# Performance work log

Hardware: AMD Instinct MI355X
Metric: run time of the kernel (lower is better)

Reference implementation:

```python
import jax, jax.numpy as jnp
import numpy as np

B, N, D = 32, 2048, 1024


def setup_inputs() -> dict:
    key = jax.random.key(0)
    k1, k2, k3, k4, k5, k6 = jax.random.split(key, 6)
    encoded = jax.random.normal(k1, (B, N, D), dtype=jnp.float32)
    decoder_state = jax.random.normal(k2, (B, D), dtype=jnp.float32)
    mask = jax.random.randint(k3, (B, N), 0, 2, dtype=jnp.int32)
    scale = 1.0 / np.sqrt(D)
    W1 = jax.random.normal(k4, (D, D), dtype=jnp.float32) * scale  # applied as x @ W1
    W2 = jax.random.normal(k5, (D, D), dtype=jnp.float32) * scale
    vt = jax.random.normal(k6, (D,), dtype=jnp.float32) * scale
    return {"encoded": encoded, "decoder_state": decoder_state, "mask": mask,
            "W1": W1, "W2": W2, "vt": vt}


def reference(encoded, decoder_state, mask, W1, W2, vt):
    temperature = 1.0
    # process_encoded: W1(encoded)  [B, N, D]
    enc = jnp.einsum('bnd,de->bne', encoded, W1)
    # W2(decoder_state)  [B, D] -> broadcast-add over N
    dec = decoder_state @ W2
    # vt(tanh(.)).squeeze(2)  -> logits [B, N]
    u = jnp.einsum('bnd,d->bn', jnp.tanh(enc + dec[:, None, :]), vt)
    # masked log-softmax with temperature over dim=1
    logits = u / temperature + jnp.log(mask.astype(u.dtype) + 1e-45)
    return jax.nn.log_softmax(logits, axis=1)
```

## Files before the change

### kernel.cpp

```cpp
#include <hip/hip_runtime.h>

typedef _Float16 half8 __attribute__((ext_vector_type(8)));
typedef _Float16 half4 __attribute__((ext_vector_type(4)));
typedef __fp16   pk2   __attribute__((ext_vector_type(2)));
typedef float    f32x4 __attribute__((ext_vector_type(4)));

#define GLOBAL_AS __attribute__((address_space(1)))
#define LDS_AS    __attribute__((address_space(3)))

static constexpr int Bb = 32;
static constexpr int Nn = 2048;
static constexpr int Dd = 1024;
static constexpr int M  = Bb * Nn;


__global__ void prep_w1(const float* __restrict__ W1, _Float16* __restrict__ W1TT) {
    int g = blockIdx.x * 256 + threadIdx.x;
    int chunk = g >> 10;
    int u = g & 1023;
    int q = u >> 7, sc = u & 127;
    int cl = sc ^ (2 * (q & 3));
    int et = chunk >> 5, t = (chunk >> 1) & 15, h = chunk & 1;
    int e  = et * 256 + h * 128 + cl;
    int k0 = t * 64 + q * 8;
    half8 hh;
#pragma unroll
    for (int j = 0; j < 8; ++j)
        hh[j] = (_Float16)W1[(size_t)(k0 + j) * Dd + e];
    *(half8*)(W1TT + (size_t)g * 8) = hh;
}

__global__ void dec_kernel(const float* __restrict__ ds, const float* __restrict__ W2,
                           float* __restrict__ dec) {
    __shared__ float part[4][64];
    int b = blockIdx.x, ech = blockIdx.y;
    int tid = threadIdx.x;
    int e = ech * 64 + (tid & 63);
    int dc = tid >> 6;
    float acc = 0.f;
#pragma unroll 4
    for (int d = dc * 256; d < dc * 256 + 256; ++d)
        acc += ds[b * Dd + d] * W2[(size_t)d * Dd + e];
    part[dc][tid & 63] = acc;
    __syncthreads();
    if (tid < 64)
        dec[b * Dd + e] = part[0][tid] + part[1][tid] + part[2][tid] + part[3][tid];
}

#define BAR     asm volatile("s_barrier" ::: "memory")
#define LGKM(n) asm volatile("s_waitcnt lgkmcnt(" #n ")" ::: "memory")
#define VM(n)   asm volatile("s_waitcnt vmcnt(" #n ")" ::: "memory")
#define PRIO1   __builtin_amdgcn_s_setprio(1)
#define PRIO0   __builtin_amdgcn_s_setprio(0)

#define RD_A(dst, base) do { _Pragma("unroll") \
  for (int ks = 0; ks < 2; ++ks) { \
    _Pragma("unroll") for (int m2 = 0; m2 < 4; ++m2) { \
      const int row_ = m2 * 32 + rA; \
      const int kc0_ = (ks * 4 + qq) * 2; \
      dst[m2][ks] = *(const half8*)&lds[(base) + (row_ * 16 + (kc0_ ^ rxa)) * 4]; \
    } } } while (0)

#define RD_B(dst, base) do { _Pragma("unroll") \
  for (int ks = 0; ks < 2; ++ks) { const int qb = ((ks * 4 + qq) * 128) * 8; \
    _Pragma("unroll") for (int j2 = 0; j2 < 2; ++j2) \
      dst[j2][ks] = *(const half8*)&lds[(base) + qb + (j2 * 64 + rB) * 8]; } } while (0)

#define MFMAQ(A_, B_, ro, co) do { \
  _Pragma("unroll") for (int m2 = 0; m2 < 4; ++m2) \
  _Pragma("unroll") for (int j2 = 0; j2 < 2; ++j2) { \
    acc[(ro) + m2][(co) + j2] = __builtin_amdgcn_mfma_f32_16x16x32_f16( \
        A_[m2][0], B_[j2][0], acc[(ro) + m2][(co) + j2], 0, 0, 0); \
    acc[(ro) + m2][(co) + j2] = __builtin_amdgcn_mfma_f32_16x16x32_f16( \
        A_[m2][1], B_[j2][1], acc[(ro) + m2][(co) + j2], 0, 0, 0); } } while (0)

__global__ __launch_bounds__(512, 2) void gemm8(
    const float* __restrict__ encA, const _Float16* __restrict__ W1TT,
    const float* __restrict__ dec, const float* __restrict__ vt,
    float* __restrict__ u_part)
{
    extern __shared__ _Float16 lds[];

    const int g  = blockIdx.x;
    const int wg = (g & 7) * 128 + (g >> 3);
    const int et    = wg & 3;
    const int mtile = wg >> 2;

    const int tid  = threadIdx.x;
    const int lane = tid & 63, wid = tid >> 6;
    const int wr = wid >> 2, wc = wid & 3;
    const int qq = lane >> 4, l15 = lane & 15;
    const int l15s = l15 ^ (2 * qq);
    const int rA = wr * 16 + l15;
    const int rxa = (l15 & 7) * 2;
    const int rB = wc * 16 + l15s;

    f32x4 acc[8][4] = {};
    half8 a[4][2], b0[2][2], b1[2][2];
    f32x4 aSt[8];

    const int arow0 = tid >> 4;
    const int l16   = tid & 15;
    const float* agp = encA + (((size_t)(mtile * 256 + arow0)) << 10) + l16 * 4;

    const size_t bbase = (size_t)et * 32 * 8192;
    const int uoff = tid * 8;

    auto issueA = [&](int T) {
        const float* gp = agp + T * 64;
#pragma unroll
        for (int p = 0; p < 8; ++p)
            aSt[p] = *(const f32x4*)(gp + ((size_t)p << 15));
    };
    auto writeA = [&](int Tn) {
        const int base = (Tn & 1) << 14;
#pragma unroll
        for (int p = 0; p < 8; ++p) {
            const int rf = p * 32 + arow0;
            const int h  = rf >> 7, row = rf & 127;
            pk2 c0 = __builtin_amdgcn_cvt_pkrtz(aSt[p][0], aSt[p][1]);
            pk2 c1 = __builtin_amdgcn_cvt_pkrtz(aSt[p][2], aSt[p][3]);
            half4 hh; hh[0] = c0[0]; hh[1] = c0[1]; hh[2] = c1[0]; hh[3] = c1[1];
            *(half4*)&lds[base + h * 8192
                          + (row * 16 + (l16 ^ ((row & 7) * 2))) * 4] = hh;
        }
    };
    auto stB = [&](int T, int h) {
        const _Float16* gp = W1TT + bbase + ((size_t)(T * 2 + h) << 13) + uoff;
        _Float16* lp = lds + (32768 + (((T & 1) * 2 + h) << 13) + (wid << 9));
        __builtin_amdgcn_global_load_lds((const GLOBAL_AS void*)gp,
                                         (LDS_AS void*)lp, 16, 0, 0);
        __builtin_amdgcn_global_load_lds((const GLOBAL_AS void*)(gp + 4096),
                                         (LDS_AS void*)(lp + 4096), 16, 0, 0);
    };


    issueA(0); stB(0, 0); stB(0, 1);
    VM(4);
    writeA(0);
    VM(0); LGKM(0);
    BAR;

#pragma unroll 2
    for (int T = 0; T < 16; ++T) {
        const int As  = (T & 1) << 14;
        const int Bs2 = 32768 + ((T & 1) << 14);
        const bool s = (T < 15);

        if (s) { issueA(T + 1); stB(T + 1, 0); stB(T + 1, 1); }

        RD_A(a, As);
        RD_B(b0, Bs2);
        RD_B(b1, Bs2 + 8192);
        LGKM(4);
        PRIO1; MFMAQ(a, b0, 0, 0); PRIO0;
        LGKM(0);
        PRIO1; MFMAQ(a, b1, 0, 2); PRIO0;
        RD_A(a, As + 8192);
        LGKM(0);
        PRIO1; MFMAQ(a, b0, 4, 0); MFMAQ(a, b1, 4, 2); PRIO0;

        if (s) { VM(4); writeA(T + 1); }
        VM(0); LGKM(0);
        BAR;
    }

    const int b = mtile >> 3;
    float vtv[4], dcv[4];
#pragma unroll
    for (int nf = 0; nf < 4; ++nf) {
        int e = et * 256 + (nf >> 1) * 128 + (nf & 1) * 64 + wc * 16 + l15;
        vtv[nf] = vt[e];
        dcv[nf] = dec[b * Dd + e];
    }
    float* usum = (float*)lds;
#pragma unroll
    for (int hm = 0; hm < 8; ++hm) {
        const int h = hm >> 2, mq = hm & 3;
#pragma unroll
        for (int r = 0; r < 4; ++r) {
            float sv = 0.f;
#pragma unroll
            for (int nf = 0; nf < 4; ++nf) {
                float x  = acc[hm][nf][r] + dcv[nf];
                float ex = __expf(2.f * x);
                sv += (1.f - 2.f * __builtin_amdgcn_rcpf(ex + 1.f)) * vtv[nf];
            }
#pragma unroll
            for (int off = 1; off < 16; off <<= 1) sv += __shfl_xor(sv, off, 16);
            if (l15 == 0)
                usum[wc * 256 + h * 128 + mq * 32 + wr * 16 + qq * 4 + r] = sv;
        }
    }
    __syncthreads();
    if (tid < 256) {
        float v = usum[tid] + usum[256 + tid] + usum[512 + tid] + usum[768 + tid];
        u_part[(size_t)et * M + (size_t)mtile * 256 + tid] = v;
    }
}

__global__ void softmax_k(const float* __restrict__ up, const int* __restrict__ mask,
                          float* __restrict__ out) {
    __shared__ float red[8];
    int b = blockIdx.x, tid = threadIdx.x;
    float l[8];
#pragma unroll
    for (int i = 0; i < 8; ++i) {
        int n = i * 256 + tid;
        float s = up[(size_t)b * Nn + n];
#pragma unroll
        for (int et = 1; et < 4; ++et) s += up[(size_t)et * M + (size_t)b * Nn + n];
        l[i] = s + (mask[b * Nn + n] ? 0.f : -103.278931f);
    }
    float m = l[0];
#pragma unroll
    for (int i = 1; i < 8; ++i) m = fmaxf(m, l[i]);
#pragma unroll
    for (int o = 32; o >= 1; o >>= 1) m = fmaxf(m, __shfl_xor(m, o, 64));
    if ((tid & 63) == 0) red[tid >> 6] = m;
    __syncthreads();
    m = fmaxf(fmaxf(red[0], red[1]), fmaxf(red[2], red[3]));
    float s = 0.f;
#pragma unroll
    for (int i = 0; i < 8; ++i) s += expf(l[i] - m);
#pragma unroll
    for (int o = 32; o >= 1; o >>= 1) s += __shfl_xor(s, o, 64);
    if ((tid & 63) == 0) red[4 + (tid >> 6)] = s;
    __syncthreads();
    float lse = m + logf(red[4] + red[5] + red[6] + red[7]);
#pragma unroll
    for (int i = 0; i < 8; ++i)
        out[(size_t)b * Nn + i * 256 + tid] = l[i] - lse;
}

extern "C" void kernel_launch(void* const* d_in, const int* in_sizes, int n_in,
                              void* d_out, int out_size, void* d_ws, size_t ws_size,
                              hipStream_t stream) {
    const float* encoded = (const float*)d_in[0];
    const float* dstate  = (const float*)d_in[1];
    const int*   mask    = (const int*)d_in[2];
    const float* W1      = (const float*)d_in[3];
    const float* W2      = (const float*)d_in[4];
    const float* vt      = (const float*)d_in[5];
    float* out = (float*)d_out;

    char* ws = (char*)d_ws;
    float*    u_part = (float*)ws;
    float*    dec    = (float*)(ws + (size_t)4 * M * 4);
    _Float16* W1TT   = (_Float16*)(ws + (size_t)4 * M * 4 + (size_t)Bb * Dd * 4);

    static bool attr_done = false;
    if (!attr_done) {
        hipFuncSetAttribute(reinterpret_cast<const void*>(gemm8),
                            hipFuncAttributeMaxDynamicSharedMemorySize, 131072);
        attr_done = true;
    }

    prep_w1<<<512, 256, 0, stream>>>(W1, W1TT);
    dec_kernel<<<dim3(32, 16), 256, 0, stream>>>(dstate, W2, dec);
    gemm8<<<1024, 512, 131072, stream>>>(encoded, W1TT, dec, vt, u_part);
    softmax_k<<<32, 256, 0, stream>>>(u_part, mask, out);
}
```

Baseline: 523.7 us.

## Split A-tile staging into two halves to cut registers and overlap with MFMA

The fp32 A-tile prefetch is split into two halves of four vectors each. The first half is written to LDS mid-iteration, and the second half is issued then, overlapping with the second MFMA group. This halves the staging registers, which may relieve register pressure. Loop unrolling drops from 2 to 1, and sched_barriers pin the ordering. The cost is more wait points per iteration and less latency hiding for the second half of the load.

Result: slower. 541.5 us (+3.4%).

```diff
diff --git a/kernel.cpp b/kernel.cpp
--- a/kernel.cpp
+++ b/kernel.cpp
@@ -97,7 +97,7 @@
 
     f32x4 acc[8][4] = {};
     half8 a[4][2], b0[2][2], b1[2][2];
-    f32x4 aSt[8];
+    f32x4 aSt[4];
 
     const int arow0 = tid >> 4;
     const int l16   = tid & 15;
@@ -106,23 +106,21 @@
     const size_t bbase = (size_t)et * 32 * 8192;
     const int uoff = tid * 8;
 
-    auto issueA = [&](int T) {
-        const float* gp = agp + T * 64;
-#pragma unroll
-        for (int p = 0; p < 8; ++p)
+    auto issueA = [&](int T, int h) {
+        const float* gp = agp + T * 64 + ((size_t)h << 17);
+#pragma unroll
+        for (int p = 0; p < 4; ++p)
             aSt[p] = *(const f32x4*)(gp + ((size_t)p << 15));
     };
-    auto writeA = [&](int Tn) {
-        const int base = (Tn & 1) << 14;
-#pragma unroll
-        for (int p = 0; p < 8; ++p) {
-            const int rf = p * 32 + arow0;
-            const int h  = rf >> 7, row = rf & 127;
+    auto writeA = [&](int Tn, int h) {
+        const int base = ((Tn & 1) << 14) + h * 8192;
+#pragma unroll
+        for (int p = 0; p < 4; ++p) {
+            const int row = p * 32 + arow0;
             pk2 c0 = __builtin_amdgcn_cvt_pkrtz(aSt[p][0], aSt[p][1]);
             pk2 c1 = __builtin_amdgcn_cvt_pkrtz(aSt[p][2], aSt[p][3]);
             half4 hh; hh[0] = c0[0]; hh[1] = c0[1]; hh[2] = c1[0]; hh[3] = c1[1];
-            *(half4*)&lds[base + h * 8192
-                          + (row * 16 + (l16 ^ ((row & 7) * 2))) * 4] = hh;
+            *(half4*)&lds[base + (row * 16 + (l16 ^ ((row & 7) * 2))) * 4] = hh;
         }
     };
     auto stB = [&](int T, int h) {
@@ -135,19 +133,21 @@
     };
 
 
-    issueA(0); stB(0, 0); stB(0, 1);
-    VM(4);
-    writeA(0);
-    VM(0); LGKM(0);
+    issueA(0, 0); stB(0, 0); stB(0, 1);
+    VM(4);  writeA(0, 0);
+    __builtin_amdgcn_sched_barrier(0);
+    issueA(0, 1);
+    VM(0);  writeA(0, 1);
+    LGKM(0);
     BAR;
 
-#pragma unroll 2
+#pragma unroll 1
     for (int T = 0; T < 16; ++T) {
         const int As  = (T & 1) << 14;
         const int Bs2 = 32768 + ((T & 1) << 14);
         const bool s = (T < 15);
 
-        if (s) { issueA(T + 1); stB(T + 1, 0); stB(T + 1, 1); }
+        if (s) { issueA(T + 1, 0); stB(T + 1, 0); stB(T + 1, 1); }
 
         RD_A(a, As);
         RD_B(b0, Bs2);
@@ -157,11 +157,20 @@
         LGKM(0);
         PRIO1; MFMAQ(a, b1, 0, 2); PRIO0;
         RD_A(a, As + 8192);
+        if (s) {
+            VM(4);
+            writeA(T + 1, 0);
+            __builtin_amdgcn_sched_barrier(0);
+            issueA(T + 1, 1);
+            LGKM(4);
+        } else {
+            LGKM(0);
+        }
+        PRIO1; MFMAQ(a, b0, 4, 0); MFMAQ(a, b1, 4, 2); PRIO0;
+
+        VM(0);
+        if (s) writeA(T + 1, 1);
         LGKM(0);
-        PRIO1; MFMAQ(a, b0, 4, 0); MFMAQ(a, b1, 4, 2); PRIO0;
-
-        if (s) { VM(4); writeA(T + 1); }
-        VM(0); LGKM(0);
         BAR;
     }
 
```
